# Optimization experiments

Hardware: AMD Instinct MI355X
Metric: run time of the kernel (lower is better)

Reference implementation:

```python
import jax, jax.numpy as jnp
import numpy as np

E = 1024      # embed_dim
H = 16        # num_heads
D = E // H    # head_dim
F = 4096      # ff_dim
EPS = 1e-5


def setup_inputs() -> dict:
    key = jax.random.key(0)
    ks = jax.random.split(key, 12)
    s = 0.02
    return {
        "x": jax.random.normal(ks[0], (2, 2048, E), dtype=jnp.float32),
        "qkv_w": jax.random.normal(ks[1], (3 * E, E), dtype=jnp.float32) * s,
        "qkv_b": jnp.zeros((3 * E,), dtype=jnp.float32),
        "out_w": jax.random.normal(ks[2], (E, E), dtype=jnp.float32) * s,
        "out_b": jnp.zeros((E,), dtype=jnp.float32),
        "ff1_w": jax.random.normal(ks[3], (F, E), dtype=jnp.float32) * s,
        "ff1_b": jnp.zeros((F,), dtype=jnp.float32),
        "ff2_w": jax.random.normal(ks[4], (E, F), dtype=jnp.float32) * s,
        "ff2_b": jnp.zeros((E,), dtype=jnp.float32),
        "ln1_g": jnp.ones((E,), dtype=jnp.float32),
        "ln1_b": jnp.zeros((E,), dtype=jnp.float32),
        "ln2_g": jnp.ones((E,), dtype=jnp.float32),
        "ln2_b": jnp.zeros((E,), dtype=jnp.float32),
    }


def _layernorm(x, g, b):
    mu = jnp.mean(x, axis=-1, keepdims=True)
    var = jnp.mean(jnp.square(x - mu), axis=-1, keepdims=True)
    return (x - mu) * jax.lax.rsqrt(var + EPS) * g + b


def reference(x, qkv_w, qkv_b, out_w, out_b, ff1_w, ff1_b, ff2_w, ff2_b,
              ln1_g, ln1_b, ln2_g, ln2_b):
    B, S, _ = x.shape
    scale = D ** -0.5

    # --- attention sublayer (pre-LN) ---
    h = _layernorm(x, ln1_g, ln1_b)
    qkv = h @ qkv_w.T + qkv_b                          # [B,S,3E]
    qkv = qkv.reshape(B, S, 3, H, D)
    q, k, v = qkv[:, :, 0], qkv[:, :, 1], qkv[:, :, 2]  # [B,S,H,D]
    scores = jnp.einsum("bqhd,bkhd->bhqk", q, k) * scale
    attn = jax.nn.softmax(scores, axis=-1)
    o = jnp.einsum("bhqk,bkhd->bqhd", attn, v).reshape(B, S, E)
    x = x + o @ out_w.T + out_b

    # --- FFN sublayer (pre-LN, exact GELU) ---
    h = _layernorm(x, ln2_g, ln2_b)
    h = jax.nn.gelu(h @ ff1_w.T + ff1_b, approximate=False)
    x = x + h @ ff2_w.T + ff2_b
    return x
```

## Files before the change

kernel.cpp:

```cpp
#include <hip/hip_runtime.h>
#include <math.h>


typedef __attribute__((ext_vector_type(8))) short short8;
typedef __attribute__((ext_vector_type(4))) float f32x4;

__device__ __forceinline__ unsigned short f2bf(float f) {
  unsigned int u = __float_as_uint(f);
  u += 0x7fffu + ((u >> 16) & 1u);
  return (unsigned short)(u >> 16);
}

__device__ __forceinline__ float fexp2(float x) {
  return __builtin_amdgcn_exp2f(x);
}

__device__ __forceinline__ short8 pack8(float4 a, float4 b) {
  short8 p;
  p[0] = (short)f2bf(a.x); p[1] = (short)f2bf(a.y);
  p[2] = (short)f2bf(a.z); p[3] = (short)f2bf(a.w);
  p[4] = (short)f2bf(b.x); p[5] = (short)f2bf(b.y);
  p[6] = (short)f2bf(b.z); p[7] = (short)f2bf(b.w);
  return p;
}

__device__ __forceinline__ float gelu_fast(float v) {
  float g = 0.7978845608f * fmaf(0.044715f * v, v * v, v);
  float den = 1.0f + fexp2(-2.885390082f * g);
  return v * __builtin_amdgcn_rcpf(den);
}

__device__ __forceinline__ void async16(const void* g, void* l) {
  __builtin_amdgcn_global_load_lds(
      (const __attribute__((address_space(1))) unsigned int*)g,
      (__attribute__((address_space(3))) unsigned int*)l, 16, 0, 0);
}

__global__ __launch_bounds__(256) void conv_all(
    const float* __restrict__ i0, unsigned short* __restrict__ o0, int n0,
    const float* __restrict__ i1, unsigned short* __restrict__ o1, int n1,
    const float* __restrict__ i2, unsigned short* __restrict__ o2, int n2,
    const float* __restrict__ i3, unsigned short* __restrict__ o3, int n3) {
  int i = blockIdx.x * 256 + threadIdx.x;
  const float* in; unsigned short* out;
  if (i < n0) { in = i0; out = o0; }
  else if ((i -= n0) < n1) { in = i1; out = o1; }
  else if ((i -= n1) < n2) { in = i2; out = o2; }
  else { i -= n2; in = i3; out = o3; if (i >= n3) return; }
  float4 v = ((const float4*)in)[i];
  ushort4 u;
  u.x = f2bf(v.x); u.y = f2bf(v.y); u.z = f2bf(v.z); u.w = f2bf(v.w);
  ((ushort4*)out)[i] = u;
}

__global__ __launch_bounds__(256) void ln_kernel(const float* __restrict__ x,
                                                 const float* __restrict__ g,
                                                 const float* __restrict__ b,
                                                 unsigned short* __restrict__ out) {
  int row = blockIdx.x;
  int t = threadIdx.x;
  const float4* x4 = (const float4*)(x + (size_t)row * 1024);
  float4 v = x4[t];
  float s1 = v.x + v.y + v.z + v.w;
  float s2 = v.x * v.x + v.y * v.y + v.z * v.z + v.w * v.w;
  for (int off = 1; off < 64; off <<= 1) {
    s1 += __shfl_xor(s1, off, 64);
    s2 += __shfl_xor(s2, off, 64);
  }
  __shared__ float r1[4], r2[4];
  int w = t >> 6, lane = t & 63;
  if (lane == 0) { r1[w] = s1; r2[w] = s2; }
  __syncthreads();
  s1 = r1[0] + r1[1] + r1[2] + r1[3];
  s2 = r2[0] + r2[1] + r2[2] + r2[3];
  float mu = s1 * (1.0f / 1024.0f);
  float var = s2 * (1.0f / 1024.0f) - mu * mu;
  float rstd = rsqrtf(var + 1e-5f);
  int c = t * 4;
  float4 gv = ((const float4*)g)[t];
  float4 bv = ((const float4*)b)[t];
  unsigned short* o = out + (size_t)row * 1024 + c;
  o[0] = f2bf((v.x - mu) * rstd * gv.x + bv.x);
  o[1] = f2bf((v.y - mu) * rstd * gv.y + bv.y);
  o[2] = f2bf((v.z - mu) * rstd * gv.z + bv.z);
  o[3] = f2bf((v.w - mu) * rstd * gv.w + bv.w);
}

template <int MODE, int BM, int BN, int BK, int LIN, int NW>
__global__ __launch_bounds__(NW * 64) void gemm_bt(
    const unsigned short* __restrict__ A, const unsigned short* __restrict__ W,
    const float* __restrict__ bias, int M, int N, int K,
    const float* __restrict__ resid, float* __restrict__ out_f32,
    unsigned short* __restrict__ out_bf16,
    unsigned short* __restrict__ qbp, unsigned short* __restrict__ kbp,
    unsigned short* __restrict__ vtb) {
  constexpr int MI = BM / 32;
  constexpr int WCOLS = (NW == 8) ? 4 : 2;
  constexpr int CW = BN / WCOLS;
  constexpr int NJ = CW / 16;
  constexpr int LPR = BK / 8;
  constexpr int RPW = 512 / BK;
  constexpr int RRND = NW * RPW;
  constexpr int NIA = BM / RRND;
  constexpr int NIW = BN / RRND;
  constexpr int KK = BK / 32;
  static_assert(MODE != 0 || (NW == 4 && BN == 128), "MODE 0 epilogue assumes NW=4/BN=128");
  static_assert(MODE != 2 || CW == 64, "MODE 2 pack path assumes CW=64");
  __shared__ __attribute__((aligned(16))) unsigned short As[2][BM * BK];
  __shared__ __attribute__((aligned(16))) unsigned short Ws[2][BN * BK];
  int tid = threadIdx.x;
  int w = tid >> 6, lane = tid & 63, quad = lane >> 4, l16 = lane & 15;
  int wrow = w / WCOLS, wcol = w % WCOLS;
  int m0, n0;
  if (LIN) {
    int id = blockIdx.x;
    int mc = M / BM;
    m0 = (id % mc) * BM;
    n0 = (id / mc) * BN;
  } else {
    m0 = blockIdx.y * BM;
    n0 = blockIdx.x * BN;
  }

  int srow = lane / LPR;
  int sseg = lane % LPR;
  int ssw = (BK == 64) ? (srow & 7) : ((srow >> 1) & 3);
  int scol = (sseg ^ ssw) * 8;
  const unsigned short* Ag = A + (size_t)(m0 + w * RPW + srow) * K + scol;
  const unsigned short* Wg = W + (size_t)(n0 + w * RPW + srow) * K + scol;

  f32x4 acc[MI][NJ] = {};

  for (int i = 0; i < NIA; i++)
    async16(Ag + (size_t)(i * RRND) * K, As[0] + (i * RRND + w * RPW) * BK);
  for (int i = 0; i < NIW; i++)
    async16(Wg + (size_t)(i * RRND) * K, Ws[0] + (i * RRND + w * RPW) * BK);

  int fsw = (BK == 64) ? (l16 & 7) : ((l16 >> 1) & 3);

  for (int k0 = 0; k0 < K; k0 += BK) {
    int buf = (k0 / BK) & 1;
    __syncthreads();
    if (k0 + BK < K) {
      int nb = buf ^ 1;
      for (int i = 0; i < NIA; i++)
        async16(Ag + (size_t)(i * RRND) * K + k0 + BK, As[nb] + (i * RRND + w * RPW) * BK);
      for (int i = 0; i < NIW; i++)
        async16(Wg + (size_t)(i * RRND) * K + k0 + BK, Ws[nb] + (i * RRND + w * RPW) * BK);
    }
    if constexpr (MI >= 8) {
      for (int kk = 0; kk < KK; kk++) {
        short8 bfr[NJ];
        for (int j = 0; j < NJ; j++)
          bfr[j] = *(const short8*)(Ws[buf] + (wcol * CW + j * 16 + l16) * BK +
                                    ((kk * 4 + quad) ^ fsw) * 8);
        for (int i = 0; i < MI; i++) {
          short8 afr = *(const short8*)(As[buf] + (wrow * (BM / 2) + i * 16 + l16) * BK +
                                        ((kk * 4 + quad) ^ fsw) * 8);
          for (int j = 0; j < NJ; j++)
            acc[i][j] = __builtin_amdgcn_mfma_f32_16x16x32_bf16(afr, bfr[j], acc[i][j], 0, 0, 0);
        }
      }
    } else {
      short8 af[MI][KK], bf[NJ][KK];
      for (int i = 0; i < MI; i++)
        for (int kk = 0; kk < KK; kk++)
          af[i][kk] = *(const short8*)(As[buf] + (wrow * (BM / 2) + i * 16 + l16) * BK +
                                       ((kk * 4 + quad) ^ fsw) * 8);
      for (int j = 0; j < NJ; j++)
        for (int kk = 0; kk < KK; kk++)
          bf[j][kk] = *(const short8*)(Ws[buf] + (wcol * CW + j * 16 + l16) * BK +
                                       ((kk * 4 + quad) ^ fsw) * 8);
      for (int kk = 0; kk < KK; kk++)
        for (int i = 0; i < MI; i++)
          for (int j = 0; j < NJ; j++)
            acc[i][j] = __builtin_amdgcn_mfma_f32_16x16x32_bf16(af[i][kk], bf[j][kk], acc[i][j], 0, 0, 0);
    }
  }

  __syncthreads();
  constexpr int EPF = 16 * CW;
  float* ep = (w < NW / 2) ? ((float*)As + w * EPF)
                           : ((float*)Ws + (w - NW / 2) * EPF);
  int orow = lane >> 2;
  int oseg = lane & 3;
  int colbase = n0 + wcol * CW;
  float bv[NJ];
  for (int j = 0; j < NJ; j++) bv[j] = bias[colbase + j * 16 + l16];

  if (MODE == 1 || MODE == 2) {
    for (int i = 0; i < MI; i++) {
      for (int j = 0; j < NJ; j++)
        for (int r = 0; r < 4; r++) {
          int row = quad * 4 + r, col = j * 16 + l16;
          float v = acc[i][j][r] + bv[j];
          if (MODE == 2) v = gelu_fast(v);
          ep[row * CW + (((col >> 2) ^ (row & 7)) << 2) + (col & 3)] = v;
        }
      asm volatile("s_waitcnt lgkmcnt(0)" ::: "memory");
      int grow = m0 + wrow * (BM / 2) + i * 16 + orow;
      if (MODE == 1) {
        for (int t = 0; t < CW / 16; t++) {
          int sl = t * 4 + oseg;
          float4 v = *(float4*)(ep + orow * CW + ((sl ^ (orow & 7)) << 2));
          const float4 rv = *(const float4*)(resid + (size_t)grow * N + colbase + sl * 4);
          v.x += rv.x; v.y += rv.y; v.z += rv.z; v.w += rv.w;
          *(float4*)(out_f32 + (size_t)grow * N + colbase + sl * 4) = v;
        }
      } else {
        for (int t = 0; t < 2; t++) {
          int s0 = t * 8 + oseg * 2;
          float4 a = *(float4*)(ep + orow * 64 + ((s0 ^ (orow & 7)) << 2));
          float4 b = *(float4*)(ep + orow * 64 + (((s0 + 1) ^ (orow & 7)) << 2));
          *(short8*)(out_bf16 + (size_t)grow * N + colbase + t * 32 + oseg * 8) = pack8(a, b);
        }
      }
      asm volatile("s_waitcnt lgkmcnt(0)" ::: "memory");
    }
  } else {
    int whichW = colbase >> 10;
    int hh = (colbase & 1023) >> 6;
    int bh = (m0 >> 11) * 16 + hh;
    int sbase = (m0 & 2047) + wrow * (BM / 2);
    if (whichW < 2) {
      unsigned short* dst0 = (whichW == 0) ? qbp : kbp;
      float qs = (whichW == 0) ? 0.1803368801f : 1.0f;
      for (int i = 0; i < MI; i++) {
        for (int j = 0; j < NJ; j++)
          for (int r = 0; r < 4; r++) {
            int row = quad * 4 + r, col = j * 16 + l16;
            ep[row * 64 + (((col >> 2) ^ (row & 7)) << 2) + (col & 3)] =
                (acc[i][j][r] + bv[j]) * qs;
          }
        asm volatile("s_waitcnt lgkmcnt(0)" ::: "memory");
        int s = sbase + i * 16 + orow;
        for (int t = 0; t < 2; t++) {
          int s0 = t * 8 + oseg * 2;
          float4 a = *(float4*)(ep + orow * 64 + ((s0 ^ (orow & 7)) << 2));
          float4 b = *(float4*)(ep + orow * 64 + (((s0 + 1) ^ (orow & 7)) << 2));
          *(short8*)(dst0 + ((size_t)bh * 2048 + s) * 64 + t * 32 + oseg * 8) = pack8(a, b);
        }
        asm volatile("s_waitcnt lgkmcnt(0)" ::: "memory");
      }
    } else {
      for (int j = 0; j < NJ; j++) {
        for (int i = 0; i < MI; i++) {
          float4 v4;
          v4.x = acc[i][j][0] + bv[j];
          v4.y = acc[i][j][1] + bv[j];
          v4.z = acc[i][j][2] + bv[j];
          v4.w = acc[i][j][3] + bv[j];
          *(float4*)(ep + l16 * 64 + (((i * 4 + quad) ^ (l16 & 7)) << 2)) = v4;
        }
        asm volatile("s_waitcnt lgkmcnt(0)" ::: "memory");
        int d = j * 16 + orow;
        for (int t = 0; t < 2; t++) {
          int s0 = t * 8 + oseg * 2;
          float4 a = *(float4*)(ep + orow * 64 + ((s0 ^ (orow & 7)) << 2));
          float4 b = *(float4*)(ep + orow * 64 + (((s0 + 1) ^ (orow & 7)) << 2));
          *(short8*)(vtb + ((size_t)bh * 64 + d) * 2048 + sbase + t * 32 + oseg * 8) = pack8(a, b);
        }
        asm volatile("s_waitcnt lgkmcnt(0)" ::: "memory");
      }
    }
  }
}

#define ALDP 72

__global__ __launch_bounds__(512) void attn_kernel(const unsigned short* __restrict__ qb,
                                                   const unsigned short* __restrict__ kb,
                                                   const unsigned short* __restrict__ vtb,
                                                   unsigned short* __restrict__ ob) {
  __shared__ __attribute__((aligned(16))) unsigned short Ks[2][64 * 64];
  __shared__ __attribute__((aligned(16))) unsigned short Vs[2][64 * 64];
  __shared__ __attribute__((aligned(16))) unsigned short Ps[8][16 * ALDP];

  int tid = threadIdx.x;
  int w = tid >> 6, lane = tid & 63, quad = lane >> 4, l16 = lane & 15;
  int bi = blockIdx.x;
  int bh = (bi & 7) * 4 + ((bi >> 3) & 3);
  int q0 = (bi >> 5) * 128 + w * 16;

  const unsigned short* qbase = qb + ((size_t)bh * 2048 + q0) * 64;
  const unsigned short* kbase = kb + (size_t)bh * 2048 * 64;
  const unsigned short* vbase = vtb + (size_t)bh * 64 * 2048;
  unsigned short* Pw = Ps[w];

  int srow = lane >> 3;
  int scol = ((lane & 7) ^ srow) * 8;
  const unsigned short* kg0 = kbase + (size_t)(w * 8 + srow) * 64 + scol;
  const unsigned short* vg0 = vbase + (size_t)(w * 8 + srow) * 2048 + scol;

  short8 qf[2];
  qf[0] = *(const short8*)(qbase + l16 * 64 + quad * 8);
  qf[1] = *(const short8*)(qbase + l16 * 64 + 32 + quad * 8);

  float lsum = 0.0f;
  f32x4 oacc[4] = {};
  int sw = l16 & 7;

  async16(kg0, &Ks[0][(w * 8) * 64]);
  async16(vg0, &Vs[0][(w * 8) * 64]);

  for (int c0 = 0; c0 < 2048; c0 += 64) {
    int buf = (c0 >> 6) & 1;
    __syncthreads();
    if (c0 + 64 < 2048) {
      int nb = buf ^ 1;
      async16(kg0 + (size_t)(c0 + 64) * 64, &Ks[nb][(w * 8) * 64]);
      async16(vg0 + c0 + 64, &Vs[nb][(w * 8) * 64]);
    }
    short8 kf[4][2];
    for (int t = 0; t < 4; t++) {
      const unsigned short* kr = &Ks[buf][(t * 16 + l16) * 64];
      kf[t][0] = *(const short8*)(kr + (quad ^ sw) * 8);
      kf[t][1] = *(const short8*)(kr + ((4 + quad) ^ sw) * 8);
    }
    f32x4 s[4];
    for (int t = 0; t < 4; t++) {
      f32x4 z = {0.0f, 0.0f, 0.0f, 0.0f};
      z = __builtin_amdgcn_mfma_f32_16x16x32_bf16(kf[t][0], qf[0], z, 0, 0, 0);
      z = __builtin_amdgcn_mfma_f32_16x16x32_bf16(kf[t][1], qf[1], z, 0, 0, 0);
      s[t] = z;
    }
    float rsum = 0.0f;
    unsigned short* pr = Pw + l16 * ALDP;
    for (int t = 0; t < 4; t++) {
      float p0 = fexp2(s[t][0]);
      float p1 = fexp2(s[t][1]);
      float p2 = fexp2(s[t][2]);
      float p3 = fexp2(s[t][3]);
      rsum += (p0 + p1) + (p2 + p3);
      uint2 pk;
      pk.x = __builtin_amdgcn_perm(__float_as_uint(p1), __float_as_uint(p0), 0x07060302u);
      pk.y = __builtin_amdgcn_perm(__float_as_uint(p3), __float_as_uint(p2), 0x07060302u);
      *(uint2*)(pr + t * 16 + quad * 4) = pk;
    }
    rsum += __shfl_xor(rsum, 16, 64);
    rsum += __shfl_xor(rsum, 32, 64);
    lsum += rsum;
    asm volatile("s_waitcnt lgkmcnt(0)" ::: "memory");
    for (int ks = 0; ks < 2; ks++) {
      short8 af = *(const short8*)(Pw + l16 * ALDP + ks * 32 + quad * 8);
      for (int j = 0; j < 4; j++) {
        short8 vf = *(const short8*)(&Vs[buf][(j * 16 + l16) * 64] +
                                     ((ks * 4 + quad) ^ sw) * 8);
        oacc[j] = __builtin_amdgcn_mfma_f32_16x16x32_bf16(af, vf, oacc[j], 0, 0, 0);
      }
    }
  }

  float linv[4];
  for (int r = 0; r < 4; r++)
    linv[r] = __builtin_amdgcn_rcpf(__shfl(lsum, quad * 4 + r, 64));
  int bb = bh >> 4, hh = bh & 15;
  for (int j = 0; j < 4; j++)
    for (int r = 0; r < 4; r++) {
      size_t tok = (size_t)bb * 2048 + q0 + quad * 4 + r;
      ob[tok * 1024 + hh * 64 + j * 16 + l16] = f2bf(oacc[j][r] * linv[r]);
    }
}

extern "C" void kernel_launch(void* const* d_in, const int* in_sizes, int n_in,
                              void* d_out, int out_size, void* d_ws, size_t ws_size,
                              hipStream_t stream) {
  (void)in_sizes; (void)n_in; (void)out_size; (void)ws_size;
  const float* x     = (const float*)d_in[0];
  const float* qkv_w = (const float*)d_in[1];
  const float* qkv_b = (const float*)d_in[2];
  const float* out_w = (const float*)d_in[3];
  const float* out_b = (const float*)d_in[4];
  const float* ff1_w = (const float*)d_in[5];
  const float* ff1_b = (const float*)d_in[6];
  const float* ff2_w = (const float*)d_in[7];
  const float* ff2_b = (const float*)d_in[8];
  const float* ln1_g = (const float*)d_in[9];
  const float* ln1_b = (const float*)d_in[10];
  const float* ln2_g = (const float*)d_in[11];
  const float* ln2_b = (const float*)d_in[12];
  float* out = (float*)d_out;
  char* ws = (char*)d_ws;

  const int M = 4096;

  unsigned short* WQ = (unsigned short*)(ws + 0);
  unsigned short* WO = (unsigned short*)(ws + 6291456);
  unsigned short* W1 = (unsigned short*)(ws + 8388608);
  unsigned short* W2 = (unsigned short*)(ws + 16777216);
  unsigned short* Hb = (unsigned short*)(ws + 25165824);
  unsigned short* Qb = (unsigned short*)(ws + 33554432);
  unsigned short* Kb = (unsigned short*)(ws + 41943040);
  unsigned short* VT = (unsigned short*)(ws + 50331648);
  unsigned short* Ob = (unsigned short*)(ws + 58720256);
  float*          X1 = (float*)(ws + 67108864);
  unsigned short* Gb = (unsigned short*)(ws + 33554432);

  conv_all<<<12288, 256, 0, stream>>>(qkv_w, WQ, 786432, out_w, WO, 262144,
                                      ff1_w, W1, 1048576, ff2_w, W2, 1048576);

  ln_kernel<<<4096, 256, 0, stream>>>(x, ln1_g, ln1_b, Hb);

  gemm_bt<0, 128, 128, 64, 0, 4><<<dim3(24, 32), 256, 0, stream>>>(
      Hb, WQ, qkv_b, M, 3072, 1024, nullptr, nullptr, nullptr, Qb, Kb, VT);

  attn_kernel<<<512, 512, 0, stream>>>(Qb, Kb, VT, Ob);

  gemm_bt<1, 64, 128, 64, 1, 8><<<512, 512, 0, stream>>>(
      Ob, WO, out_b, M, 1024, 1024, x, X1, nullptr, nullptr, nullptr, nullptr);

  ln_kernel<<<4096, 256, 0, stream>>>(X1, ln2_g, ln2_b, Hb);

  gemm_bt<2, 256, 256, 64, 0, 8><<<dim3(16, 16), 512, 0, stream>>>(
      Hb, W1, ff1_b, M, 4096, 1024, nullptr, nullptr, Gb, nullptr, nullptr, nullptr);

  gemm_bt<1, 64, 128, 64, 1, 8><<<512, 512, 0, stream>>>(
      Gb, W2, ff2_b, M, 1024, 4096, X1, out, nullptr, nullptr, nullptr, nullptr);
}
```

Before: 325.4 us.

## Add triple-buffered register-double-buffered GEMM for out-proj and FF2 with residual

Adds a new 128x128 tile GEMM kernel with a three-stage async LDS pipeline and ping-pong register fragment sets, so LDS reads for the next k-step overlap the MFMAs of the current one. The kernel fuses bias and residual add in a swizzled LDS epilogue. It replaces the previous 64x128 gemm_bt instantiation for the output projection and FF2. The larger tiles give 256 blocks on 256 CUs, which means fewer waves and less latency hiding, and the double fragment sets raise register use.

```diff
diff --git a/kernel.cpp b/kernel.cpp
--- a/kernel.cpp
+++ b/kernel.cpp
@@ -266,6 +266,122 @@
   }
 }
 
+struct FragSet {
+  short8 a[4][2];
+  short8 b[4][2];
+};
+
+__global__ __launch_bounds__(256) void gemm_sk(
+    const unsigned short* __restrict__ A, const unsigned short* __restrict__ W,
+    const float* __restrict__ bias, int M, int N, int K,
+    const float* __restrict__ resid, float* __restrict__ out_f32) {
+  __shared__ __attribute__((aligned(16))) unsigned short As[3][128 * 64];
+  __shared__ __attribute__((aligned(16))) unsigned short Ws[3][128 * 64];
+  int tid = threadIdx.x;
+  int w = tid >> 6, lane = tid & 63, quad = lane >> 4, l16 = lane & 15;
+  int wrow = w >> 1, wcol = w & 1;
+  int id = blockIdx.x;
+  int mc = M / 128;
+  int m0 = (id % mc) * 128;
+  int n0 = (id / mc) * 128;
+
+  int srow = lane >> 3;
+  int sseg = lane & 7;
+  int scol = (sseg ^ (srow & 7)) * 8;
+  const unsigned short* Ag = A + (size_t)(m0 + w * 8 + srow) * K + scol;
+  const unsigned short* Wg = W + (size_t)(n0 + w * 8 + srow) * K + scol;
+  int fsw = l16 & 7;
+  int nk = K >> 6;
+
+  f32x4 acc[4][4] = {};
+
+#define SK_STAGE(kt)                                                         \
+  {                                                                          \
+    int _b = (kt) % 3;                                                       \
+    int _ko = (kt) << 6;                                                     \
+    for (int i = 0; i < 4; i++)                                              \
+      async16(Ag + (size_t)(i * 32) * K + _ko, As[_b] + (i * 32 + w * 8) * 64); \
+    for (int i = 0; i < 4; i++)                                              \
+      async16(Wg + (size_t)(i * 32) * K + _ko, Ws[_b] + (i * 32 + w * 8) * 64); \
+  }
+
+#define SK_READ(kt, F)                                                       \
+  {                                                                          \
+    int _b = (kt) % 3;                                                       \
+    for (int i = 0; i < 4; i++)                                              \
+      for (int kk = 0; kk < 2; kk++)                                         \
+        F.a[i][kk] = *(const short8*)(As[_b] + (wrow * 64 + i * 16 + l16) * 64 + \
+                                      ((kk * 4 + quad) ^ fsw) * 8);          \
+    for (int j = 0; j < 4; j++)                                              \
+      for (int kk = 0; kk < 2; kk++)                                         \
+        F.b[j][kk] = *(const short8*)(Ws[_b] + (wcol * 64 + j * 16 + l16) * 64 + \
+                                      ((kk * 4 + quad) ^ fsw) * 8);          \
+  }
+
+#define SK_MFMA(F)                                                           \
+  for (int kk = 0; kk < 2; kk++)                                             \
+    for (int i = 0; i < 4; i++)                                              \
+      for (int j = 0; j < 4; j++)                                            \
+        acc[i][j] = __builtin_amdgcn_mfma_f32_16x16x32_bf16(F.a[i][kk], F.b[j][kk], acc[i][j], 0, 0, 0);
+
+#define SK_ITER(t, Fc, Fl)                                                   \
+  {                                                                          \
+    if ((t) + 2 < nk)                                                        \
+      asm volatile("s_waitcnt vmcnt(8)" ::: "memory");                       \
+    else                                                                     \
+      asm volatile("s_waitcnt vmcnt(0)" ::: "memory");                       \
+    asm volatile("s_waitcnt lgkmcnt(0)" ::: "memory");                       \
+    __builtin_amdgcn_s_barrier();                                            \
+    if ((t) + 3 < nk) SK_STAGE((t) + 3);                                     \
+    if ((t) + 1 < nk) SK_READ((t) + 1, Fl);                                  \
+    SK_MFMA(Fc);                                                             \
+  }
+
+  SK_STAGE(0);
+  SK_STAGE(1);
+  SK_STAGE(2);
+  asm volatile("s_waitcnt vmcnt(16)" ::: "memory");
+  __builtin_amdgcn_s_barrier();
+
+  FragSet fA, fB;
+  SK_READ(0, fA);
+
+  for (int t = 0; t < nk; t += 2) {
+    SK_ITER(t, fA, fB);
+    SK_ITER(t + 1, fB, fA);
+  }
+#undef SK_ITER
+#undef SK_MFMA
+#undef SK_READ
+#undef SK_STAGE
+
+  __syncthreads();
+  float* ep = (w < 2) ? ((float*)As + w * 1024) : ((float*)Ws + (w - 2) * 1024);
+  int orow = lane >> 2;
+  int oseg = lane & 3;
+  int colbase = n0 + wcol * 64;
+  float bv[4];
+  for (int j = 0; j < 4; j++) bv[j] = bias[colbase + j * 16 + l16];
+
+  for (int i = 0; i < 4; i++) {
+    for (int j = 0; j < 4; j++)
+      for (int r = 0; r < 4; r++) {
+        int row = quad * 4 + r, col = j * 16 + l16;
+        ep[row * 64 + (((col >> 2) ^ (row & 7)) << 2) + (col & 3)] = acc[i][j][r] + bv[j];
+      }
+    asm volatile("s_waitcnt lgkmcnt(0)" ::: "memory");
+    int grow = m0 + wrow * 64 + i * 16 + orow;
+    for (int t = 0; t < 4; t++) {
+      int sl = t * 4 + oseg;
+      float4 v = *(float4*)(ep + orow * 64 + ((sl ^ (orow & 7)) << 2));
+      const float4 rv = *(const float4*)(resid + (size_t)grow * N + colbase + sl * 4);
+      v.x += rv.x; v.y += rv.y; v.z += rv.z; v.w += rv.w;
+      *(float4*)(out_f32 + (size_t)grow * N + colbase + sl * 4) = v;
+    }
+    asm volatile("s_waitcnt lgkmcnt(0)" ::: "memory");
+  }
+}
+
 #define ALDP 72
 
 __global__ __launch_bounds__(512) void attn_kernel(const unsigned short* __restrict__ qb,
@@ -406,14 +522,12 @@
 
   attn_kernel<<<512, 512, 0, stream>>>(Qb, Kb, VT, Ob);
 
-  gemm_bt<1, 64, 128, 64, 1, 8><<<512, 512, 0, stream>>>(
-      Ob, WO, out_b, M, 1024, 1024, x, X1, nullptr, nullptr, nullptr, nullptr);
+  gemm_sk<<<256, 256, 0, stream>>>(Ob, WO, out_b, M, 1024, 1024, x, X1);
 
   ln_kernel<<<4096, 256, 0, stream>>>(X1, ln2_g, ln2_b, Hb);
 
   gemm_bt<2, 256, 256, 64, 0, 8><<<dim3(16, 16), 512, 0, stream>>>(
       Hb, W1, ff1_b, M, 4096, 1024, nullptr, nullptr, Gb, nullptr, nullptr, nullptr);
 
-  gemm_bt<1, 64, 128, 64, 1, 8><<<512, 512, 0, stream>>>(
-      Gb, W2, ff2_b, M, 1024, 4096, X1, out, nullptr, nullptr, nullptr, nullptr);
-}
+  gemm_sk<<<256, 256, 0, stream>>>(Gb, W2, ff2_b, M, 1024, 4096, X1, out);
+}
```

Measured after the change: 343.4 us. +5.5%, slower.
